# Performance work log

Hardware: AMD Instinct MI355X
Metric: run time of the kernel (lower is better)

Reference implementation:

```python
import jax, jax.numpy as jnp
import numpy as np

N_NODES = 50000
N_EDGES = 600000
N_LABEL = 200000
IN_CH = 128
OUT_CH = 128
K_HOPS = 2


def setup_inputs() -> dict:
    key = jax.random.key(0)
    ks = jax.random.split(key, 9)
    x = jax.random.normal(ks[0], (N_NODES, IN_CH), dtype=jnp.float32)
    edge_index = jax.random.randint(ks[1], (2, N_EDGES), 0, N_NODES)
    edge_label_index = jax.random.randint(ks[2], (2, N_LABEL), 0, N_NODES)
    conv_weight = jax.random.normal(ks[3], (OUT_CH, IN_CH), dtype=jnp.float32) * 0.05
    conv_bias = jax.random.normal(ks[4], (OUT_CH,), dtype=jnp.float32) * 0.05
    w1 = jax.random.normal(ks[5], (OUT_CH // 2, OUT_CH), dtype=jnp.float32) * 0.05
    b1 = jax.random.normal(ks[6], (OUT_CH // 2,), dtype=jnp.float32) * 0.05
    w2 = jax.random.normal(ks[7], (1, OUT_CH // 2), dtype=jnp.float32) * 0.05
    b2 = jax.random.normal(ks[8], (1,), dtype=jnp.float32) * 0.05
    return {"x": x, "edge_index": edge_index, "edge_label_index": edge_label_index,
            "conv_weight": conv_weight, "conv_bias": conv_bias,
            "w1": w1, "b1": b1, "w2": w2, "b2": b2}


def reference(x, edge_index, edge_label_index, conv_weight, conv_bias, w1, b1, w2, b2):
    n = x.shape[0]
    # gcn_norm with self-loops: A_hat = D^{-1/2} (A + I) D^{-1/2}
    loop = jnp.arange(n, dtype=edge_index.dtype)
    src = jnp.concatenate([edge_index[0], loop])  # message sources
    dst = jnp.concatenate([edge_index[1], loop])  # aggregation targets
    deg = jax.ops.segment_sum(jnp.ones_like(dst, dtype=x.dtype), dst, num_segments=n)
    dinv = jnp.where(deg > 0, jax.lax.rsqrt(deg), 0.0)
    w = dinv[src] * dinv[dst]  # [E+N] edge weights

    # K-hop propagation: h <- A_hat h, repeated K times (SGConv)
    h = x
    for _ in range(K_HOPS):
        h = jax.ops.segment_sum(h[src] * w[:, None], dst, num_segments=n)
    z = h @ conv_weight.T + conv_bias  # [N, out_channels]

    # decode: gather endpoint embeddings, multiply, tiny MLP (dropout inactive at eval)
    s = z[edge_label_index[0]] * z[edge_label_index[1]]  # [E_label, out]
    h1 = jax.nn.relu(s @ w1.T + b1)
    r = (h1 @ w2.T + b2).sum(axis=-1)  # [E_label]
    return r
```

## Files before the change

### kernel.cpp

```cpp
#include <hip/hip_runtime.h>

#define N_CH 128
#define SLOT 64

typedef _Float16 half8  __attribute__((ext_vector_type(8)));
typedef _Float16 half4v __attribute__((ext_vector_type(4)));
typedef float    floatx4 __attribute__((ext_vector_type(4)));
typedef unsigned int uint4v __attribute__((ext_vector_type(4)));


__global__ void k_prep(int* __restrict__ cur,
                       const float* __restrict__ W,  _Float16* __restrict__ wh,
                       const float* __restrict__ W1, _Float16* __restrict__ w1h,
                       int n) {
    int i = blockIdx.x * blockDim.x + threadIdx.x;
    if (i < n) cur[i] = 0;
    int nw4  = N_CH * N_CH / 4;
    int nw14 = 64 * N_CH / 4;
    if (i < nw4) {
        float4 v = ((const float4*)W)[i];
        half4v o;
        o[0] = (_Float16)v.x; o[1] = (_Float16)v.y; o[2] = (_Float16)v.z; o[3] = (_Float16)v.w;
        ((half4v*)wh)[i] = o;
    } else if (i < nw4 + nw14) {
        int j = i - nw4;
        float4 v = ((const float4*)W1)[j];
        half4v o;
        o[0] = (_Float16)v.x; o[1] = (_Float16)v.y; o[2] = (_Float16)v.z; o[3] = (_Float16)v.w;
        ((half4v*)w1h)[j] = o;
    }
}


__global__ void k_fillfix(const int* __restrict__ src, const int* __restrict__ dst,
                          int* __restrict__ cur, unsigned short* __restrict__ csr, int E) {
    int e = blockIdx.x * blockDim.x + threadIdx.x;
    if (e < E) {
        int d = dst[e];
        int p = atomicAdd(&cur[d], 1);
        if (p < SLOT) csr[d * SLOT + p] = (unsigned short)src[e];
    }
}


__global__ __launch_bounds__(256) void k_metascale(
        const int* __restrict__ cur, int2* __restrict__ meta,
        unsigned short* __restrict__ csr,
        const float* __restrict__ x,
        _Float16* __restrict__ u0, _Float16* __restrict__ u1, int n) {
    int i = blockIdx.x * blockDim.x + threadIdx.x;
    int tot = n * 16;
    if (i < tot) {
        int node = i >> 4, chunk = i & 15;
        int ct = cur[node];
        float d = rsqrtf((float)(ct + 1));
        int c = (ct < SLOT) ? ct : SLOT;
        if (chunk == 0) {
            int cp = (c + 7) & ~7;
            unsigned short zn = (unsigned short)n;
            for (int j = c; j < cp; ++j) csr[node * SLOT + j] = zn;
            int2 mv; mv.x = cp >> 3; mv.y = __float_as_int(d);
            meta[node] = mv;
        }
        float4 v0 = ((const float4*)x)[node * 32 + chunk * 2];
        float4 v1 = ((const float4*)x)[node * 32 + chunk * 2 + 1];
        half8 o;
        o[0] = (_Float16)(d * v0.x); o[1] = (_Float16)(d * v0.y);
        o[2] = (_Float16)(d * v0.z); o[3] = (_Float16)(d * v0.w);
        o[4] = (_Float16)(d * v1.x); o[5] = (_Float16)(d * v1.y);
        o[6] = (_Float16)(d * v1.z); o[7] = (_Float16)(d * v1.w);
        ((half8*)u0)[node * 16 + chunk] = o;
    } else if (i < tot + 32) {
        int j = i - tot;
        _Float16* d16 = (j < 16) ? u0 : u1;
        half8 zz;
        #pragma unroll
        for (int q = 0; q < 8; ++q) zz[q] = (_Float16)0.f;
        ((half8*)d16)[n * 16 + (j & 15)] = zz;
    }
}


__global__ __launch_bounds__(256) void k_hop16(const _Float16* __restrict__ hin,
                                               _Float16* __restrict__ hout,
                                               const int2* __restrict__ meta,
                                               const unsigned short* __restrict__ csr,
                                               int n, int squared) {
    int tid = threadIdx.x;
    int node = blockIdx.x * 16 + (tid >> 4);
    if (node >= n) return;
    int c = tid & 15;
    int2 mv = meta[node];
    int nq = mv.x;
    float di = __int_as_float(mv.y);
    float sc = squared ? di * di : di;
    const uint4v* qlst = (const uint4v*)(csr + node * SLOT);
    const half8* hp = (const half8*)hin;
    half8 self = hp[node * 16 + c];
    float acc[8];
    #pragma unroll
    for (int j = 0; j < 8; ++j) acc[j] = (float)self[j];
    for (int q = 0; q < nq; ++q) {
        uint4v pk = qlst[q];
        int idx[8];
        idx[0] = pk[0] & 0xFFFF; idx[1] = pk[0] >> 16;
        idx[2] = pk[1] & 0xFFFF; idx[3] = pk[1] >> 16;
        idx[4] = pk[2] & 0xFFFF; idx[5] = pk[2] >> 16;
        idx[6] = pk[3] & 0xFFFF; idx[7] = pk[3] >> 16;
        half8 u[8];
        #pragma unroll
        for (int i = 0; i < 8; ++i)
            u[i] = hp[idx[i] * 16 + c];
        #pragma unroll
        for (int i = 0; i < 8; ++i)
            #pragma unroll
            for (int j = 0; j < 8; ++j) acc[j] += (float)u[i][j];
    }
    half8 o;
    #pragma unroll
    for (int j = 0; j < 8; ++j) o[j] = (_Float16)(sc * acc[j]);
    ((half8*)hout)[node * 16 + c] = o;
}


__global__ __launch_bounds__(256) void k_zlin_mfma(const _Float16* __restrict__ h,
                                                   const _Float16* __restrict__ wh,
                                                   const float* __restrict__ bc,
                                                   _Float16* __restrict__ z, int n) {
    __shared__ half8 wls[128 * 16];
    int tid = threadIdx.x;
    int lane = tid & 63, w = tid >> 6;
    int quad = lane >> 4, m16 = lane & 15;
    int nb = blockIdx.x * 64;
    #pragma unroll
    for (int i = 0; i < 8; ++i) {
        int g = tid + 256 * i;
        int r = g >> 4, c = g & 15;
        wls[r * 16 + (c ^ (r & 15))] = ((const half8*)wh)[g];
    }
    int arow = nb + w * 16 + m16;
    const half8* hrow = (const half8*)(h + (size_t)arow * N_CH);
    half8 a[4];
    #pragma unroll
    for (int kk = 0; kk < 4; ++kk) a[kk] = hrow[kk * 4 + quad];
    __syncthreads();
    int outnode0 = nb + w * 16 + quad * 4;
    #pragma unroll
    for (int jt = 0; jt < 8; ++jt) {
        floatx4 acc = {0.f, 0.f, 0.f, 0.f};
        #pragma unroll
        for (int kk = 0; kk < 4; ++kk) {
            int r = jt * 16 + m16;
            half8 bfr = wls[r * 16 + ((kk * 4 + quad) ^ m16)];
            acc = __builtin_amdgcn_mfma_f32_16x16x32_f16(a[kk], bfr, acc, 0, 0, 0);
        }
        int j = jt * 16 + m16;
        float bias = bc[j];
        #pragma unroll
        for (int reg = 0; reg < 4; ++reg) {
            int node = outnode0 + reg;
            if (node < n) z[(size_t)node * N_CH + j] = (_Float16)(acc[reg] + bias);
        }
    }
}


__global__ __launch_bounds__(256) void k_decode_mfma(const _Float16* __restrict__ z,
        const int* __restrict__ ai, const int* __restrict__ bi,
        const _Float16* __restrict__ w1h, const float* __restrict__ b1,
        const float* __restrict__ w2, const float* __restrict__ b2,
        float* __restrict__ out, int m) {
    __shared__ half8 w1ls[64 * 16];
    __shared__ half8 sls[64 * 16];
    int tid = threadIdx.x;
    int lane = tid & 63, w = tid >> 6;
    int quad = lane >> 4, m16 = lane & 15;
    int pbase = blockIdx.x * 64;
    #pragma unroll
    for (int i = 0; i < 4; ++i) {
        int g = tid + 256 * i;
        int r = g >> 4, c = g & 15;
        w1ls[r * 16 + (c ^ (r & 15))] = ((const half8*)w1h)[g];
    }
    int pidx = pbase + w * 16 + m16;
    if (pidx >= m) pidx = m - 1;
    int idxa = ai[pidx];
    int idxb = bi[pidx];
    int ia[4], ib[4];
    #pragma unroll
    for (int it = 0; it < 4; ++it) {
        int p = it * 4 + quad;
        ia[it] = __shfl(idxa, p, 64);
        ib[it] = __shfl(idxb, p, 64);
    }
    half8 za[4], zb[4];
    #pragma unroll
    for (int it = 0; it < 4; ++it) {
        za[it] = ((const half8*)(z + (size_t)ia[it] * N_CH))[m16];
        zb[it] = ((const half8*)(z + (size_t)ib[it] * N_CH))[m16];
    }
    #pragma unroll
    for (int it = 0; it < 4; ++it) {
        half8 s8 = za[it] * zb[it];
        int pp = w * 16 + it * 4 + quad;
        sls[pp * 16 + (m16 ^ (pp & 15))] = s8;
    }
    __syncthreads();
    half8 a[4];
    #pragma unroll
    for (int kk = 0; kk < 4; ++kk)
        a[kk] = sls[(w * 16 + m16) * 16 + ((kk * 4 + quad) ^ m16)];
    float rsum[4] = {0.f, 0.f, 0.f, 0.f};
    #pragma unroll
    for (int jt = 0; jt < 4; ++jt) {
        floatx4 acc = {0.f, 0.f, 0.f, 0.f};
        #pragma unroll
        for (int kk = 0; kk < 4; ++kk) {
            int r = jt * 16 + m16;
            half8 bfr = w1ls[r * 16 + ((kk * 4 + quad) ^ m16)];
            acc = __builtin_amdgcn_mfma_f32_16x16x32_f16(a[kk], bfr, acc, 0, 0, 0);
        }
        int j = jt * 16 + m16;
        float b1j = b1[j], w2j = w2[j];
        #pragma unroll
        for (int reg = 0; reg < 4; ++reg) {
            float v = fmaxf(acc[reg] + b1j, 0.f) * w2j;
            v += __shfl_xor(v, 1, 64);
            v += __shfl_xor(v, 2, 64);
            v += __shfl_xor(v, 4, 64);
            v += __shfl_xor(v, 8, 64);
            rsum[reg] += v;
        }
    }
    if (m16 == 0) {
        float bb = b2[0];
        #pragma unroll
        for (int reg = 0; reg < 4; ++reg) {
            int gp = pbase + w * 16 + quad * 4 + reg;
            if (gp < m) out[gp] = rsum[reg] + bb;
        }
    }
}


extern "C" void kernel_launch(void* const* d_in, const int* in_sizes, int n_in,
                              void* d_out, int out_size, void* d_ws, size_t ws_size,
                              hipStream_t stream) {
    const float* x   = (const float*)d_in[0];
    const int*   ei  = (const int*)d_in[1];
    const int*   eli = (const int*)d_in[2];
    const float* W   = (const float*)d_in[3];
    const float* bc  = (const float*)d_in[4];
    const float* W1  = (const float*)d_in[5];
    const float* b1  = (const float*)d_in[6];
    const float* w2  = (const float*)d_in[7];
    const float* b2  = (const float*)d_in[8];
    float* out = (float*)d_out;

    const int N = in_sizes[0] / N_CH;
    const int E = in_sizes[1] / 2;
    const int M = in_sizes[2] / 2;

    const int* src = ei;
    const int* dst = ei + E;
    const int* ai  = eli;
    const int* bi  = eli + M;

    _Float16* hb0 = (_Float16*)d_ws;
    _Float16* hb1 = hb0 + (size_t)(N + 1) * N_CH;
    _Float16* wh  = hb1 + (size_t)(N + 1) * N_CH;
    _Float16* w1h = wh + 16384;
    unsigned short* csr = (unsigned short*)(w1h + 8192);
    int2*  meta = (int2*)(csr + (size_t)N * SLOT + 64);
    int*   cur  = (int*)(meta + N);

    k_prep<<<(N + 255) / 256, 256, 0, stream>>>(cur, W, wh, W1, w1h, N);
    k_fillfix<<<(E + 255) / 256, 256, 0, stream>>>(src, dst, cur, csr, E);
    int mw = N * 16 + 32;
    k_metascale<<<(mw + 255) / 256, 256, 0, stream>>>(cur, meta, csr, x, hb0, hb1, N);

    int nblk = (N + 15) / 16;
    k_hop16<<<nblk, 256, 0, stream>>>(hb0, hb1, meta, csr, N, 1);
    k_hop16<<<nblk, 256, 0, stream>>>(hb1, hb0, meta, csr, N, 0);

    k_zlin_mfma<<<(N + 63) / 64, 256, 0, stream>>>(hb0, wh, bc, hb1, N);

    k_decode_mfma<<<(M + 63) / 64, 256, 0, stream>>>(hb1, ai, bi, w1h, b1, w2, b2, out, M);
}
```

Baseline: 203.8 us.

## Fuse second propagation hop into the MFMA linear layer kernel

The second SpMM hop is folded into the linear-projection kernel. Each block aggregates the neighbours of its 64 nodes into a swizzled shared-memory tile, then feeds that tile straight to the MFMA GEMM. This removes one kernel launch and the global write and re-read of the intermediate hop output. The cost is that each block now does four serial gather passes per thread group before the GEMM, with fewer blocks than the standalone hop kernel, which may reduce latency hiding for the irregular gathers.

```diff
diff --git a/kernel.cpp b/kernel.cpp
--- a/kernel.cpp
+++ b/kernel.cpp
@@ -85,7 +85,7 @@
                                                _Float16* __restrict__ hout,
                                                const int2* __restrict__ meta,
                                                const unsigned short* __restrict__ csr,
-                                               int n, int squared) {
+                                               int n) {
     int tid = threadIdx.x;
     int node = blockIdx.x * 16 + (tid >> 4);
     if (node >= n) return;
@@ -93,7 +93,7 @@
     int2 mv = meta[node];
     int nq = mv.x;
     float di = __int_as_float(mv.y);
-    float sc = squared ? di * di : di;
+    float sc = di * di;
     const uint4v* qlst = (const uint4v*)(csr + node * SLOT);
     const half8* hp = (const half8*)hin;
     half8 self = hp[node * 16 + c];
@@ -123,11 +123,14 @@
 }
 
 
-__global__ __launch_bounds__(256) void k_zlin_mfma(const _Float16* __restrict__ h,
-                                                   const _Float16* __restrict__ wh,
-                                                   const float* __restrict__ bc,
-                                                   _Float16* __restrict__ z, int n) {
+__global__ __launch_bounds__(256) void k_hopz(const _Float16* __restrict__ hin,
+                                              const int2* __restrict__ meta,
+                                              const unsigned short* __restrict__ csr,
+                                              const _Float16* __restrict__ wh,
+                                              const float* __restrict__ bc,
+                                              _Float16* __restrict__ z, int n) {
     __shared__ half8 wls[128 * 16];
+    __shared__ half8 sls[64 * 16];
     int tid = threadIdx.x;
     int lane = tid & 63, w = tid >> 6;
     int quad = lane >> 4, m16 = lane & 15;
@@ -138,12 +141,52 @@
         int r = g >> 4, c = g & 15;
         wls[r * 16 + (c ^ (r & 15))] = ((const half8*)wh)[g];
     }
-    int arow = nb + w * 16 + m16;
-    const half8* hrow = (const half8*)(h + (size_t)arow * N_CH);
+    int grp = tid >> 4;
+    int c = tid & 15;
+    const half8* hp = (const half8*)hin;
+    #pragma unroll 1
+    for (int s = 0; s < 4; ++s) {
+        int r = grp + 16 * s;
+        int node = nb + r;
+        half8 o;
+        if (node < n) {
+            int2 mv = meta[node];
+            int nq = mv.x;
+            float di = __int_as_float(mv.y);
+            const uint4v* qlst = (const uint4v*)(csr + node * SLOT);
+            half8 self = hp[node * 16 + c];
+            float acc[8];
+            #pragma unroll
+            for (int j = 0; j < 8; ++j) acc[j] = (float)self[j];
+            for (int q = 0; q < nq; ++q) {
+                uint4v pk = qlst[q];
+                int idx[8];
+                idx[0] = pk[0] & 0xFFFF; idx[1] = pk[0] >> 16;
+                idx[2] = pk[1] & 0xFFFF; idx[3] = pk[1] >> 16;
+                idx[4] = pk[2] & 0xFFFF; idx[5] = pk[2] >> 16;
+                idx[6] = pk[3] & 0xFFFF; idx[7] = pk[3] >> 16;
+                half8 u[8];
+                #pragma unroll
+                for (int i = 0; i < 8; ++i)
+                    u[i] = hp[idx[i] * 16 + c];
+                #pragma unroll
+                for (int i = 0; i < 8; ++i)
+                    #pragma unroll
+                    for (int j = 0; j < 8; ++j) acc[j] += (float)u[i][j];
+            }
+            #pragma unroll
+            for (int j = 0; j < 8; ++j) o[j] = (_Float16)(di * acc[j]);
+        } else {
+            #pragma unroll
+            for (int j = 0; j < 8; ++j) o[j] = (_Float16)0.f;
+        }
+        sls[r * 16 + (c ^ (r & 15))] = o;
+    }
+    __syncthreads();
     half8 a[4];
     #pragma unroll
-    for (int kk = 0; kk < 4; ++kk) a[kk] = hrow[kk * 4 + quad];
-    __syncthreads();
+    for (int kk = 0; kk < 4; ++kk)
+        a[kk] = sls[(w * 16 + m16) * 16 + ((kk * 4 + quad) ^ m16)];
     int outnode0 = nb + w * 16 + quad * 4;
     #pragma unroll
     for (int jt = 0; jt < 8; ++jt) {
@@ -280,10 +323,8 @@
     k_metascale<<<(mw + 255) / 256, 256, 0, stream>>>(cur, meta, csr, x, hb0, hb1, N);
 
     int nblk = (N + 15) / 16;
-    k_hop16<<<nblk, 256, 0, stream>>>(hb0, hb1, meta, csr, N, 1);
-    k_hop16<<<nblk, 256, 0, stream>>>(hb1, hb0, meta, csr, N, 0);
-
-    k_zlin_mfma<<<(N + 63) / 64, 256, 0, stream>>>(hb0, wh, bc, hb1, N);
-
-    k_decode_mfma<<<(M + 63) / 64, 256, 0, stream>>>(hb1, ai, bi, w1h, b1, w2, b2, out, M);
-}
+    k_hop16<<<nblk, 256, 0, stream>>>(hb0, hb1, meta, csr, N);
+    k_hopz<<<(N + 63) / 64, 256, 0, stream>>>(hb1, meta, csr, wh, bc, hb0, N);
+
+    k_decode_mfma<<<(M + 63) / 64, 256, 0, stream>>>(hb0, ai, bi, w1h, b1, w2, b2, out, M);
+}
```

After: 201.6 us. Within noise of the previous version (-1.1%).
